# Performance work log

Measured on AMD Instinct MI355X. Metric: run time of the kernel, lower is better.

## Reference

```python
import jax, jax.numpy as jnp
import numpy as np
from jax import lax

B, C, FH, FW = 2, 128, 96, 160
H, W = 384, 640
NH, NP = 4, 9
T = 0.5


def conv(x, w, b, groups=1):
    pad = w.shape[2] // 2
    y = lax.conv_general_dilated(x, w, (1, 1), [(pad, pad), (pad, pad)],
                                 dimension_numbers=('NCHW', 'OIHW', 'NCHW'),
                                 feature_group_count=groups)
    return y + b[None, :, None, None]


def lrelu(x):
    return jnp.where(x >= 0, x, 0.1 * x)


def resize(x, h, w):
    # torch F.interpolate(mode='bilinear', align_corners=False, antialias=False)
    return jax.image.resize(x, (x.shape[0], x.shape[1], h, w), method='linear', antialias=False)


def grid_sample(vals, gx, gy, align_corners):
    # vals: (N, Ch, Hv, Wv); gx, gy: (N, Ho, Wo) normalized coords in [-1, 1]
    # bilinear, padding_mode='border'
    N, Ch, Hv, Wv = vals.shape
    if align_corners:
        x = (gx + 1.0) * 0.5 * (Wv - 1)
        y = (gy + 1.0) * 0.5 * (Hv - 1)
    else:
        x = ((gx + 1.0) * Wv - 1.0) * 0.5
        y = ((gy + 1.0) * Hv - 1.0) * 0.5
    x = jnp.clip(x, 0.0, Wv - 1.0)
    y = jnp.clip(y, 0.0, Hv - 1.0)
    x0 = jnp.floor(x)
    y0 = jnp.floor(y)
    wx = (x - x0)[:, None]  # (N,1,Ho,Wo)
    wy = (y - y0)[:, None]
    x0i = x0.astype(jnp.int32)
    y0i = y0.astype(jnp.int32)
    x1i = jnp.minimum(x0i + 1, Wv - 1)
    y1i = jnp.minimum(y0i + 1, Hv - 1)
    flat = vals.reshape(N, Ch, Hv * Wv)
    gather = jax.vmap(lambda v, i: jnp.take(v, i, axis=1))  # (Ch,HW),(Ho,Wo)->(Ch,Ho,Wo)
    v00 = gather(flat, y0i * Wv + x0i)
    v01 = gather(flat, y0i * Wv + x1i)
    v10 = gather(flat, y1i * Wv + x0i)
    v11 = gather(flat, y1i * Wv + x1i)
    return (v00 * (1 - wx) * (1 - wy) + v01 * wx * (1 - wy)
            + v10 * (1 - wx) * wy + v11 * wx * wy)


def warp(feat, flow):
    b, c, h, w = feat.shape
    if flow.shape[2:] != (h, w):
        sh, sw = h / flow.shape[2], w / flow.shape[3]
        flow = resize(flow, h, w) * jnp.array([sw, sh], flow.dtype)[None, :, None, None]
    gy, gx = jnp.meshgrid(jnp.arange(h, dtype=jnp.float32),
                          jnp.arange(w, dtype=jnp.float32), indexing='ij')
    gxn = 2.0 * (gx[None] + flow[:, 0]) / max(w - 1, 1) - 1.0
    gyn = 2.0 * (gy[None] + flow[:, 1]) / max(h - 1, 1) - 1.0
    return grid_sample(feat, gxn, gyn, True)


def group_norm(x, g, b, groups=8, eps=1e-5):
    B_, C_, h, w = x.shape
    xr = x.reshape(B_, groups, C_ // groups, h, w)
    m = xr.mean(axis=(2, 3, 4), keepdims=True)
    v = xr.var(axis=(2, 3, 4), keepdims=True)
    xn = ((xr - m) * lax.rsqrt(v + eps)).reshape(B_, C_, h, w)
    return xn * g[None, :, None, None] + b[None, :, None, None]


def deform_attn(q, src, ow0, ob0, ow1, ob1, aw0, ab0, aw1, ab1, vw, vb, pw, pb):
    b, c, h, w = q.shape
    hd = c // NH
    off = conv(lrelu(conv(q, ow0, ob0, groups=NH)), ow1, ob1).reshape(b, NH, NP, 2, h, w)
    attn = conv(lrelu(conv(q, aw0, ab0, groups=NH)), aw1, ab1).reshape(b, NH, NP, h, w)
    attn = jax.nn.softmax(attn, axis=2)
    vals = conv(src, vw, vb).reshape(b * NH, hd, h, w)
    gy, gx = jnp.meshgrid(jnp.arange(h, dtype=jnp.float32),
                          jnp.arange(w, dtype=jnp.float32), indexing='ij')
    sx = gx[None, None, None] + off[:, :, :, 0]  # (b,NH,NP,h,w)
    sy = gy[None, None, None] + off[:, :, :, 1]
    gxn = (2.0 * sx / max(w - 1, 1) - 1.0).reshape(b * NH, NP * h, w)
    gyn = (2.0 * sy / max(h - 1, 1) - 1.0).reshape(b * NH, NP * h, w)
    samp = grid_sample(vals, gxn, gyn, False).reshape(b, NH, hd, NP, h, w)
    out = (samp * attn[:, :, None]).sum(axis=3).reshape(b, c, h, w)
    return conv(out, pw, pb)


def setup_inputs() -> dict:
    key = jax.random.key(0)
    ks = jax.random.split(key, 24)
    rn = lambda k, s, sc: jax.random.normal(k, s, jnp.float32) * sc
    # offset conv bias: 3x3 regular grid init (n_points=9), padded with zeros
    gs = 3
    base = []
    for dy in range(gs):
        for dx in range(gs):
            base += [dx - gs // 2, dy - gs // 2]
    ob1 = np.zeros(NH * NP * 2, np.float32)
    ob1[:len(base)] = np.asarray(base, np.float32)
    return {
        'feat1': rn(ks[0], (B, C, FH, FW), 1.0),
        'feat2': rn(ks[1], (B, C, FH, FW), 1.0),
        'flow_fwd': rn(ks[2], (B, 2, H, W), 3.0),
        'flow_bwd': rn(ks[3], (B, 2, H, W), 3.0),
        'edge1': jax.random.uniform(ks[4], (B, 1, H, W), jnp.float32),
        'edge2': jax.random.uniform(ks[5], (B, 1, H, W), jnp.float32),
        'fuse_w0': rn(ks[6], (C, 2 * C + 3, 3, 3), 0.02),
        'fuse_b0': jnp.zeros((C,), jnp.float32),
        'fuse_w1': rn(ks[7], (C, C, 3, 3), 0.02),
        'fuse_b1': jnp.zeros((C,), jnp.float32),
        'gn_g': jnp.ones((C,), jnp.float32),
        'gn_b': jnp.zeros((C,), jnp.float32),
        'off_w0': rn(ks[8], (C, C // NH, 3, 3), 0.02),
        'off_b0': jnp.zeros((C,), jnp.float32),
        'off_w1': rn(ks[9], (NH * NP * 2, C, 1, 1), 0.01),
        'off_b1': jnp.asarray(ob1),
        'aw_w0': rn(ks[10], (C, C // NH, 3, 3), 0.02),
        'aw_b0': jnp.zeros((C,), jnp.float32),
        'aw_w1': rn(ks[11], (NH * NP, C, 1, 1), 0.02),
        'aw_b1': jnp.zeros((NH * NP,), jnp.float32),
        'val_w': rn(ks[12], (C, C, 1, 1), 0.05),
        'val_b': jnp.zeros((C,), jnp.float32),
        'out_w': rn(ks[13], (C, C, 1, 1), 0.05),
        'out_b': jnp.zeros((C,), jnp.float32),
        'ffn_w0': rn(ks[14], (2 * C, C, 1, 1), 0.05),
        'ffn_b0': jnp.zeros((2 * C,), jnp.float32),
        'ffn_w1': rn(ks[15], (C, 2 * C, 1, 1), 0.05),
        'ffn_b1': jnp.zeros((C,), jnp.float32),
        'dec_w0': rn(ks[16], (64, C, 3, 3), 0.03),
        'dec_b0': jnp.zeros((64,), jnp.float32),
        'dec_w1': rn(ks[17], (32, 64, 3, 3), 0.05),
        'dec_b1': jnp.zeros((32,), jnp.float32),
        'dec_w2': rn(ks[18], (3, 32, 3, 3), 0.05),
        'dec_b2': jnp.zeros((3,), jnp.float32),
    }


def reference(feat1, feat2, flow_fwd, flow_bwd, edge1, edge2,
              fuse_w0, fuse_b0, fuse_w1, fuse_b1, gn_g, gn_b,
              off_w0, off_b0, off_w1, off_b1, aw_w0, aw_b0, aw_w1, aw_b1,
              val_w, val_b, out_w, out_b, ffn_w0, ffn_b0, ffn_w1, ffn_b1,
              dec_w0, dec_b0, dec_w1, dec_b1, dec_w2, dec_b2):
    b, c, fh, fw = feat1.shape
    h, w = edge1.shape[2], edge1.shape[3]
    f1w = warp(feat1, flow_fwd * T)
    f2w = warp(feat2, flow_bwd * (1.0 - T))
    e1 = resize(edge1, fh, fw)
    e2 = resize(edge2, fh, fw)
    tmap = jnp.full((b, 1, fh, fw), T, feat1.dtype)
    fused = jnp.concatenate([f1w, f2w, e1, e2, tmap], axis=1)
    x = lrelu(conv(lrelu(conv(fused, fuse_w0, fuse_b0)), fuse_w1, fuse_b1))
    source = f1w * (1.0 - T) + f2w * T
    x = x + deform_attn(group_norm(x, gn_g, gn_b), source,
                        off_w0, off_b0, off_w1, off_b1,
                        aw_w0, aw_b0, aw_w1, aw_b1,
                        val_w, val_b, out_w, out_b)
    x = x + conv(jax.nn.gelu(conv(x, ffn_w0, ffn_b0), approximate=False), ffn_w1, ffn_b1)
    x = resize(x, h, w)
    x = lrelu(conv(x, dec_w0, dec_b0))
    x = lrelu(conv(x, dec_w1, dec_b1))
    return jax.nn.sigmoid(conv(x, dec_w2, dec_b2))
```

## Files before the change

kernel.cpp:

```cpp
#include <hip/hip_runtime.h>

typedef _Float16 f16;
typedef _Float16 f16x8 __attribute__((ext_vector_type(8)));
typedef float f32x4 __attribute__((ext_vector_type(4)));

constexpr int Bn = 2, Cn = 128, FH = 96, FW = 160, Hh = 384, Wh = 640;
constexpr int HWl = FH * FW;
constexpr int NHd = 4, NPt = 9;

#define DEVINL __device__ __forceinline__

DEVINL f32x4 zero4() { f32x4 z; z[0] = 0.f; z[1] = 0.f; z[2] = 0.f; z[3] = 0.f; return z; }
DEVINL f16x8 zero8() {
  f16x8 z;
#pragma unroll
  for (int j = 0; j < 8; ++j) z[j] = (f16)0.f;
  return z;
}

template<int ACT> DEVINL float activ(float v) {
  if (ACT == 1) return v >= 0.f ? v : 0.1f * v;
  if (ACT == 2) return 0.5f * v * (1.f + erff(v * 0.70710678118654752f));
  if (ACT == 3) return 1.f / (1.f + expf(-v));
  return v;
}

struct PrepJob { const float* w; f16* wf; int Cout, cin_g, cout_g, KS, CoF, taps, blk0; };
struct PrepArgs { PrepJob j[12]; };

__global__ __launch_bounds__(256) void k_wprep_all(PrepArgs a)
{
  int jb = 0;
#pragma unroll
  for (int t = 1; t < 12; ++t) if ((int)blockIdx.x >= a.j[t].blk0) jb = t;
  PrepJob J = a.j[jb];
  int idx = (blockIdx.x - J.blk0) * 256 + threadIdx.x;
  int total = J.taps * J.KS * J.CoF * 64;
  if (idx >= total) return;
  int lane = idx & 63;
  int rest = idx >> 6;
  int cf = rest % J.CoF;
  int rest2 = rest / J.CoF;
  int ks = rest2 % J.KS;
  int tap = rest2 / J.KS;
  int co = cf * 16 + (lane & 15);
  f16x8 v = zero8();
#pragma unroll
  for (int j = 0; j < 8; ++j) {
    int cip = ks * 32 + (lane >> 4) * 8 + j;
    int cil = cip - (co / J.cout_g) * J.cin_g;
    float x = 0.f;
    if (co < J.Cout && cil >= 0 && cil < J.cin_g)
      x = J.w[((size_t)co * J.cin_g + cil) * J.taps + tap];
    v[j] = (f16)x;
  }
  *(f16x8*)&J.wf[(size_t)idx * 8] = v;
}

__global__ __launch_bounds__(256) void k_tr_h(
    const float* __restrict__ feat1, const float* __restrict__ feat2,
    f16* __restrict__ t1, f16* __restrict__ t2)
{
  int idx = blockIdx.x * blockDim.x + threadIdx.x;
  if (idx >= 2 * Bn * HWl * 8) return;
  int cq = idx & 7;
  int pix = (idx >> 3) % HWl;
  int z = idx / (8 * HWl);
  int b = z & 1;
  const float* src = (z >> 1) ? feat2 : feat1;
  f16* dst = (z >> 1) ? t2 : t1;
  int c0 = cq * 16;
  f16x8 v0, v1;
#pragma unroll
  for (int j = 0; j < 8; ++j) {
    v0[j] = (f16)src[(size_t)(b * Cn + c0 + j) * HWl + pix];
    v1[j] = (f16)src[(size_t)(b * Cn + c0 + 8 + j) * HWl + pix];
  }
  f16* dp = dst + ((size_t)b * HWl + pix) * 128 + c0;
  *(f16x8*)dp = v0;
  *(f16x8*)(dp + 8) = v1;
}

__global__ __launch_bounds__(256) void k_warp_fuse_h(
    const f16* __restrict__ t1, const f16* __restrict__ t2,
    const float* __restrict__ flowf, const float* __restrict__ flowb,
    const float* __restrict__ edge1, const float* __restrict__ edge2,
    f16* __restrict__ fused, f16* __restrict__ src)
{
  int idx = blockIdx.x * blockDim.x + threadIdx.x;
  if (idx >= Bn * HWl * 8) return;
  int cq = idx & 7;
  int pix = (idx >> 3) % HWl;
  int b = idx / (8 * HWl);
  int j = pix % FW;
  int i = pix / FW;

  const int y4 = 4 * i + 1, x4 = 4 * j + 1;
  const float* p;
  p = flowf + (size_t)((b * 2 + 0) * Hh + y4) * Wh + x4;
  float fx1 = 0.03125f * (p[0] + p[1] + p[Wh] + p[Wh + 1]);
  p = flowf + (size_t)((b * 2 + 1) * Hh + y4) * Wh + x4;
  float fy1 = 0.03125f * (p[0] + p[1] + p[Wh] + p[Wh + 1]);
  p = flowb + (size_t)((b * 2 + 0) * Hh + y4) * Wh + x4;
  float fx2 = 0.03125f * (p[0] + p[1] + p[Wh] + p[Wh + 1]);
  p = flowb + (size_t)((b * 2 + 1) * Hh + y4) * Wh + x4;
  float fy2 = 0.03125f * (p[0] + p[1] + p[Wh] + p[Wh + 1]);

  float sx1 = fminf(fmaxf((float)j + fx1, 0.f), (float)(FW - 1));
  float sy1 = fminf(fmaxf((float)i + fy1, 0.f), (float)(FH - 1));
  float sx2 = fminf(fmaxf((float)j + fx2, 0.f), (float)(FW - 1));
  float sy2 = fminf(fmaxf((float)i + fy2, 0.f), (float)(FH - 1));

  int x10 = (int)floorf(sx1), y10 = (int)floorf(sy1);
  int x11 = min(x10 + 1, FW - 1), y11 = min(y10 + 1, FH - 1);
  float wx1 = sx1 - (float)x10, wy1 = sy1 - (float)y10;
  int x20 = (int)floorf(sx2), y20 = (int)floorf(sy2);
  int x21 = min(x20 + 1, FW - 1), y21 = min(y20 + 1, FH - 1);
  float wx2 = sx2 - (float)x20, wy2 = sy2 - (float)y20;

  float a00 = (1.f - wx1) * (1.f - wy1), a01 = wx1 * (1.f - wy1);
  float a10 = (1.f - wx1) * wy1,         a11 = wx1 * wy1;
  float c00 = (1.f - wx2) * (1.f - wy2), c01 = wx2 * (1.f - wy2);
  float c10 = (1.f - wx2) * wy2,         c11 = wx2 * wy2;

  int c0 = cq * 16;
  const f16* b1 = t1 + (size_t)b * HWl * 128 + c0;
  const f16* b2 = t2 + (size_t)b * HWl * 128 + c0;
  const f16x8* p100 = (const f16x8*)&b1[(size_t)(y10 * FW + x10) * 128];
  const f16x8* p101 = (const f16x8*)&b1[(size_t)(y10 * FW + x11) * 128];
  const f16x8* p110 = (const f16x8*)&b1[(size_t)(y11 * FW + x10) * 128];
  const f16x8* p111 = (const f16x8*)&b1[(size_t)(y11 * FW + x11) * 128];
  const f16x8* p200 = (const f16x8*)&b2[(size_t)(y20 * FW + x20) * 128];
  const f16x8* p201 = (const f16x8*)&b2[(size_t)(y20 * FW + x21) * 128];
  const f16x8* p210 = (const f16x8*)&b2[(size_t)(y21 * FW + x20) * 128];
  const f16x8* p211 = (const f16x8*)&b2[(size_t)(y21 * FW + x21) * 128];

  f16* fp = fused + ((size_t)b * HWl + pix) * 288;
  f16* sp = src + ((size_t)b * HWl + pix) * 128;

#pragma unroll
  for (int h = 0; h < 2; ++h) {
    f16x8 u00 = p100[h], u01 = p101[h], u10 = p110[h], u11 = p111[h];
    f16x8 w00 = p200[h], w01 = p201[h], w10 = p210[h], w11 = p211[h];
    f16x8 r1, r2, rs;
#pragma unroll
    for (int k = 0; k < 8; ++k) {
      float v1 = (float)u00[k] * a00 + (float)u01[k] * a01
               + (float)u10[k] * a10 + (float)u11[k] * a11;
      float v2 = (float)w00[k] * c00 + (float)w01[k] * c01
               + (float)w10[k] * c10 + (float)w11[k] * c11;
      r1[k] = (f16)v1; r2[k] = (f16)v2; rs[k] = (f16)(0.5f * (v1 + v2));
    }
    *(f16x8*)(fp + c0 + h * 8) = r1;
    *(f16x8*)(fp + 128 + c0 + h * 8) = r2;
    *(f16x8*)(sp + c0 + h * 8) = rs;
  }

  if (cq == 0) {
    p = edge1 + (size_t)(b * Hh + y4) * Wh + x4;
    float e1v = 0.25f * (p[0] + p[1] + p[Wh] + p[Wh + 1]);
    p = edge2 + (size_t)(b * Hh + y4) * Wh + x4;
    float e2v = 0.25f * (p[0] + p[1] + p[Wh] + p[Wh + 1]);
    fp[256] = (f16)e1v;
    fp[257] = (f16)e2v;
    fp[258] = (f16)0.5f;
#pragma unroll
    for (int c = 259; c < 288; ++c) fp[c] = (f16)0.f;
  }
}

template<int ACT, int UP, int NF>
__global__ __launch_bounds__(256) void k_conv3m(
    const f16* __restrict__ Xin, const f16* __restrict__ Wf,
    const float* __restrict__ bias, f16* __restrict__ Out,
    int KS, int CoF, int Cs_in, int Cs_out, int Wd, int Ht,
    int in_r0, int in_rows, int out_r0, int out_rows, int ogr0, int ogr1)
{
  __shared__ f16 sA[8160];
  int tid = threadIdx.x;
  int wv = tid >> 6, lane = tid & 63;
  int l15 = lane & 15, l4 = lane >> 4;
  int colTiles = Wd >> 5;
  int tileC = blockIdx.x % colTiles, tileR = blockIdx.x / colTiles;
  int b = blockIdx.z;
  int co0 = blockIdx.y * (NF * 16);
  int cfB = blockIdx.y * NF;
  int rowBaseOut = ogr0 + tileR * 4;
  int rowBase = rowBaseOut - 1;
  int colBase = tileC * 32;

  f32x4 acc[2][NF];
#pragma unroll
  for (int mf = 0; mf < 2; ++mf)
#pragma unroll
    for (int nf = 0; nf < NF; ++nf) acc[mf][nf] = zero4();

  f16x8 stv[4];
  f16x8 stc[4][4];

  auto prefetch = [&](int cs) {
#pragma unroll
    for (int k = 0; k < 4; ++k) {
      int u = tid + k * 256;
      if (u < 816) {
        int s = u & 3;
        int pxy = u >> 2;
        int x = pxy % 34, y = pxy / 34;
        int gy = rowBase + y, gx = colBase + x - 1;
        if (UP) {
          stc[k][0] = zero8(); stc[k][1] = zero8();
          stc[k][2] = zero8(); stc[k][3] = zero8();
          if (gy >= 0 && gy < Ht && gx >= 0 && gx < Wd) {
            float uy = ((float)gy + 0.5f) * 0.25f - 0.5f;
            uy = fminf(fmaxf(uy, 0.f), (float)(FH - 1));
            int y0 = (int)floorf(uy);
            int y1 = min(y0 + 1, FH - 1);
            float ux = ((float)gx + 0.5f) * 0.25f - 0.5f;
            ux = fminf(fmaxf(ux, 0.f), (float)(FW - 1));
            int x0 = (int)floorf(ux);
            int x1 = min(x0 + 1, FW - 1);
            const f16* xb = Xin + (size_t)b * HWl * 128 + cs * 32 + s * 8;
            stc[k][0] = *(const f16x8*)&xb[(size_t)(y0 * FW + x0) * 128];
            stc[k][1] = *(const f16x8*)&xb[(size_t)(y0 * FW + x1) * 128];
            stc[k][2] = *(const f16x8*)&xb[(size_t)(y1 * FW + x0) * 128];
            stc[k][3] = *(const f16x8*)&xb[(size_t)(y1 * FW + x1) * 128];
          }
        } else {
          stv[k] = zero8();
          if (gy >= in_r0 && gy < in_r0 + in_rows && gx >= 0 && gx < Wd)
            stv[k] = *(const f16x8*)&Xin[(((size_t)b * in_rows + (gy - in_r0)) * Wd + gx) * Cs_in
                                         + cs * 32 + s * 8];
        }
      }
    }
  };

  auto writeLDS = [&]() {
#pragma unroll
    for (int k = 0; k < 4; ++k) {
      int u = tid + k * 256;
      if (u < 816) {
        int s = u & 3;
        int pxy = u >> 2;
        f16x8 v;
        if (UP) {
          int x = pxy % 34, y = pxy / 34;
          int gy = rowBase + y, gx = colBase + x - 1;
          float uy = ((float)gy + 0.5f) * 0.25f - 0.5f;
          uy = fminf(fmaxf(uy, 0.f), (float)(FH - 1));
          float fy = uy - floorf(uy);
          float ux = ((float)gx + 0.5f) * 0.25f - 0.5f;
          ux = fminf(fmaxf(ux, 0.f), (float)(FW - 1));
          float fx = ux - floorf(ux);
#pragma unroll
          for (int jj = 0; jj < 8; ++jj) {
            float t0 = (float)stc[k][0][jj] * (1.f - fx) + (float)stc[k][1][jj] * fx;
            float t1 = (float)stc[k][2][jj] * (1.f - fx) + (float)stc[k][3][jj] * fx;
            v[jj] = (f16)(t0 * (1.f - fy) + t1 * fy);
          }
        } else {
          v = stv[k];
        }
        *(f16x8*)((char*)sA + pxy * 80 + s * 16) = v;
      }
    }
  };

  prefetch(0);
  for (int cs = 0; cs < KS; ++cs) {
    writeLDS();
    __syncthreads();
    if (cs + 1 < KS) prefetch(cs + 1);
#pragma unroll
    for (int ky = 0; ky < 3; ++ky) {
#pragma unroll
      for (int kx = 0; kx < 3; ++kx) {
        const char* ab = (const char*)sA;
        f16x8 a0 = *(const f16x8*)(ab + ((wv + ky) * 34 + l15 + kx) * 80 + l4 * 16);
        f16x8 a1 = *(const f16x8*)(ab + ((wv + ky) * 34 + l15 + 16 + kx) * 80 + l4 * 16);
        int tap = ky * 3 + kx;
#pragma unroll
        for (int nf = 0; nf < NF; ++nf) {
          f16x8 bf = *(const f16x8*)&Wf[((((size_t)tap * KS + cs) * CoF + cfB + nf) * 64 + lane) * 8];
          acc[0][nf] = __builtin_amdgcn_mfma_f32_16x16x32_f16(a0, bf, acc[0][nf], 0, 0, 0);
          acc[1][nf] = __builtin_amdgcn_mfma_f32_16x16x32_f16(a1, bf, acc[1][nf], 0, 0, 0);
        }
      }
    }
    __syncthreads();
  }

  int r = rowBaseOut + wv;
  if (r < ogr1) {
    size_t rowoff = ((size_t)b * out_rows + (r - out_r0)) * Wd;
#pragma unroll
    for (int nf = 0; nf < NF; ++nf) {
      int co = co0 + nf * 16 + l15;
      float bv = bias[co];
#pragma unroll
      for (int mf = 0; mf < 2; ++mf) {
        int xo = colBase + mf * 16 + l4 * 4;
#pragma unroll
        for (int rg = 0; rg < 4; ++rg) {
          float v = activ<ACT>(acc[mf][nf][rg] + bv);
          Out[(rowoff + xo + rg) * Cs_out + co] = (f16)v;
        }
      }
    }
  }
}

template<int ACT, int RES>
__global__ __launch_bounds__(256) void k_gemm1x1(
    const f16* __restrict__ X, const f16* __restrict__ Wf,
    const float* __restrict__ bias, f16* __restrict__ Out,
    int KS, int CoF, int Cs_in, int Cs_out, int Cr, int coTiles, int pixTiles)
{
  int wid = blockIdx.x * 4 + (threadIdx.x >> 6);
  int lane = threadIdx.x & 63;
  int total = pixTiles * coTiles;
  if (wid >= total) return;
  int coT = wid % coTiles;
  int pixT = wid / coTiles;
  int nfc = min(4, CoF - coT * 4);
  int l15 = lane & 15, l4 = lane >> 4;

  f32x4 acc[2][4];
#pragma unroll
  for (int mf = 0; mf < 2; ++mf)
#pragma unroll
    for (int nf = 0; nf < 4; ++nf) acc[mf][nf] = zero4();

  int pA0 = pixT * 32 + l15;
  for (int ks = 0; ks < KS; ++ks) {
    f16x8 a0 = *(const f16x8*)&X[(size_t)pA0 * Cs_in + ks * 32 + l4 * 8];
    f16x8 a1 = *(const f16x8*)&X[(size_t)(pA0 + 16) * Cs_in + ks * 32 + l4 * 8];
#pragma unroll
    for (int nf = 0; nf < 4; ++nf) {
      if (nf < nfc) {
        f16x8 bf = *(const f16x8*)&Wf[(((size_t)ks * CoF + coT * 4 + nf) * 64 + lane) * 8];
        acc[0][nf] = __builtin_amdgcn_mfma_f32_16x16x32_f16(a0, bf, acc[0][nf], 0, 0, 0);
        acc[1][nf] = __builtin_amdgcn_mfma_f32_16x16x32_f16(a1, bf, acc[1][nf], 0, 0, 0);
      }
    }
  }
#pragma unroll
  for (int nf = 0; nf < 4; ++nf) {
    if (nf < nfc) {
      int co = coT * 64 + nf * 16 + l15;
      if (co < Cr) {
        float bv = bias[co];
#pragma unroll
        for (int mf = 0; mf < 2; ++mf) {
          int p0 = pixT * 32 + mf * 16 + l4 * 4;
#pragma unroll
          for (int rg = 0; rg < 4; ++rg) {
            float v = activ<ACT>(acc[mf][nf][rg] + bv);
            size_t o = (size_t)(p0 + rg) * Cs_out + co;
            if (RES) v += (float)Out[o];
            Out[o] = (f16)v;
          }
        }
      }
    }
  }
}

__global__ __launch_bounds__(256) void k_gn_part_h(
    const f16* __restrict__ X, float* __restrict__ part)
{
  int s = blockIdx.x & 7;
  int g = (blockIdx.x >> 3) & 7;
  int b = blockIdx.x >> 6;
  int tid = threadIdx.x;
  const f16* Xp = X + (size_t)b * HWl * 128 + g * 16 + (tid & 1) * 8;
  float sum = 0.f, ss = 0.f;
  for (int p = s * 1920 + (tid >> 1); p < (s + 1) * 1920; p += 128) {
    f16x8 v = *(const f16x8*)&Xp[(size_t)p * 128];
#pragma unroll
    for (int jj = 0; jj < 8; ++jj) { float f = (float)v[jj]; sum += f; ss += f * f; }
  }
  __shared__ float sh1[256], sh2[256];
  sh1[tid] = sum; sh2[tid] = ss;
  __syncthreads();
  for (int st = 128; st > 0; st >>= 1) {
    if (tid < st) { sh1[tid] += sh1[tid + st]; sh2[tid] += sh2[tid + st]; }
    __syncthreads();
  }
  if (tid == 0) {
    part[((b * 8 + g) * 8 + s) * 2] = sh1[0];
    part[((b * 8 + g) * 8 + s) * 2 + 1] = sh2[0];
  }
}

__global__ __launch_bounds__(256) void k_gn_apply_h(
    const f16* __restrict__ X, const float* __restrict__ gw,
    const float* __restrict__ gb, const float* __restrict__ part,
    f16* __restrict__ Q)
{
  int idx = blockIdx.x * blockDim.x + threadIdx.x;
  int total = Bn * HWl * 16;
  if (idx >= total) return;
  int u = idx & 15;
  int pix = (idx >> 4) % HWl;
  int b = idx / (16 * HWl);
  int c0 = u * 8;
  int g = c0 >> 4;
  const float* pp = part + ((b * 8 + g) * 8) * 2;
  float sum = 0.f, ss = 0.f;
#pragma unroll
  for (int s = 0; s < 8; ++s) { sum += pp[s * 2]; ss += pp[s * 2 + 1]; }
  const float n = 16.f * HWl;
  float mean = sum / n;
  float var = ss / n - mean * mean;
  float inv = rsqrtf(var + 1e-5f);
  f16x8 v = *(const f16x8*)&X[((size_t)b * HWl + pix) * 128 + c0];
  f16x8 r;
#pragma unroll
  for (int jj = 0; jj < 8; ++jj) {
    int c = c0 + jj;
    r[jj] = (f16)(((float)v[jj] - mean) * (gw[c] * inv) + gb[c]);
  }
  *(f16x8*)&Q[((size_t)b * HWl + pix) * 128 + c0] = r;
}

__global__ __launch_bounds__(256) void k_softmax9_h(f16* __restrict__ a)
{
  int idx = blockIdx.x * blockDim.x + threadIdx.x;
  if (idx >= Bn * NHd * HWl) return;
  int pix = idx % HWl;
  int head = (idx / HWl) & 3;
  int b = idx / (HWl * NHd);
  f16* base = a + ((size_t)b * HWl + pix) * 48 + head * 9;
  float v[9];
  float m = -1e30f;
#pragma unroll
  for (int p0 = 0; p0 < 9; ++p0) { v[p0] = (float)base[p0]; m = fmaxf(m, v[p0]); }
  float s = 0.f;
#pragma unroll
  for (int p0 = 0; p0 < 9; ++p0) { v[p0] = expf(v[p0] - m); s += v[p0]; }
  float inv = 1.f / s;
#pragma unroll
  for (int p0 = 0; p0 < 9; ++p0) base[p0] = (f16)(v[p0] * inv);
}

__global__ __launch_bounds__(256) void k_deform_h(
    const f16* __restrict__ vals, const f16* __restrict__ off,
    const f16* __restrict__ attn, f16* __restrict__ outa)
{
  int idx = blockIdx.x * blockDim.x + threadIdx.x;
  if (idx >= Bn * NHd * HWl) return;
  int pix = idx % HWl;
  int head = (idx / HWl) & 3;
  int b = idx / (HWl * NHd);
  int j = pix % FW, i = pix / FW;

  const float kx = (float)FW / (float)(FW - 1);
  const float ky = (float)FH / (float)(FH - 1);
  const f16* vb = vals + (size_t)b * HWl * 128 + head * 32;
  const f16* ab = attn + ((size_t)b * HWl + pix) * 48 + head * 9;
  const f16* ob = off + ((size_t)b * HWl + pix) * 80 + head * 18;

  float acc[32];
#pragma unroll
  for (int k = 0; k < 32; ++k) acc[k] = 0.f;

#pragma unroll
  for (int p0 = 0; p0 < 9; ++p0) {
    float ox = (float)ob[p0 * 2];
    float oy = (float)ob[p0 * 2 + 1];
    float aw = (float)ab[p0];
    float xf = ((float)j + ox) * kx - 0.5f;
    float yf = ((float)i + oy) * ky - 0.5f;
    xf = fminf(fmaxf(xf, 0.f), (float)(FW - 1));
    yf = fminf(fmaxf(yf, 0.f), (float)(FH - 1));
    int x0 = (int)floorf(xf), y0 = (int)floorf(yf);
    int x1 = min(x0 + 1, FW - 1), y1 = min(y0 + 1, FH - 1);
    float fx = xf - (float)x0, fy = yf - (float)y0;
    float w00 = aw * (1.f - fx) * (1.f - fy);
    float w01 = aw * fx * (1.f - fy);
    float w10 = aw * (1.f - fx) * fy;
    float w11 = aw * fx * fy;
    const f16x8* c00 = (const f16x8*)&vb[(size_t)(y0 * FW + x0) * 128];
    const f16x8* c01 = (const f16x8*)&vb[(size_t)(y0 * FW + x1) * 128];
    const f16x8* c10 = (const f16x8*)&vb[(size_t)(y1 * FW + x0) * 128];
    const f16x8* c11 = (const f16x8*)&vb[(size_t)(y1 * FW + x1) * 128];
#pragma unroll
    for (int k8 = 0; k8 < 4; ++k8) {
      f16x8 a = c00[k8], bb = c01[k8], cc = c10[k8], dd = c11[k8];
#pragma unroll
      for (int jj = 0; jj < 8; ++jj)
        acc[k8 * 8 + jj] += w00 * (float)a[jj] + w01 * (float)bb[jj]
                          + w10 * (float)cc[jj] + w11 * (float)dd[jj];
    }
  }
  f16* op = outa + ((size_t)b * HWl + pix) * 128 + head * 32;
#pragma unroll
  for (int k = 0; k < 32; ++k) op[k] = (f16)acc[k];
}

__global__ __launch_bounds__(256) void k_dec2_h(
    const f16* __restrict__ Xb, const float* __restrict__ w,
    const float* __restrict__ bias, float* __restrict__ out,
    int c0, int b0, int brows, int R)
{
  int idx = blockIdx.x * blockDim.x + threadIdx.x;
  if (idx >= Bn * R * Wh) return;
  int x = idx % Wh;
  int y = c0 + (idx / Wh) % R;
  int b = idx / (Wh * R);
  float a0 = bias[0], a1 = bias[1], a2 = bias[2];
#pragma unroll
  for (int ky = 0; ky < 3; ++ky) {
    int gy = y + ky - 1;
    if (gy < 0 || gy >= Hh) continue;
#pragma unroll
    for (int kxx = 0; kxx < 3; ++kxx) {
      int gx = x + kxx - 1;
      if (gx < 0 || gx >= Wh) continue;
      int tap = ky * 3 + kxx;
      const f16* px = Xb + ((size_t)(b * brows + (gy - b0)) * Wh + gx) * 32;
#pragma unroll
      for (int k8 = 0; k8 < 4; ++k8) {
        f16x8 v = *(const f16x8*)&px[k8 * 8];
#pragma unroll
        for (int jj = 0; jj < 8; ++jj) {
          int ci = k8 * 8 + jj;
          float f = (float)v[jj];
          a0 += f * w[(0 * 32 + ci) * 9 + tap];
          a1 += f * w[(1 * 32 + ci) * 9 + tap];
          a2 += f * w[(2 * 32 + ci) * 9 + tap];
        }
      }
    }
  }
  size_t o = ((size_t)(b * 3 + 0) * Hh + y) * Wh + x;
  out[o] = 1.f / (1.f + expf(-a0));
  out[o + (size_t)Hh * Wh] = 1.f / (1.f + expf(-a1));
  out[o + (size_t)2 * Hh * Wh] = 1.f / (1.f + expf(-a2));
}

extern "C" void kernel_launch(void* const* d_in, const int* in_sizes, int n_in,
                              void* d_out, int out_size, void* d_ws, size_t ws_size,
                              hipStream_t stream) {
  (void)in_sizes; (void)n_in; (void)out_size; (void)ws_size;
  const float* feat1  = (const float*)d_in[0];
  const float* feat2  = (const float*)d_in[1];
  const float* flowf  = (const float*)d_in[2];
  const float* flowb  = (const float*)d_in[3];
  const float* edge1  = (const float*)d_in[4];
  const float* edge2  = (const float*)d_in[5];
  const float* fuse_w0 = (const float*)d_in[6];
  const float* fuse_b0 = (const float*)d_in[7];
  const float* fuse_w1 = (const float*)d_in[8];
  const float* fuse_b1 = (const float*)d_in[9];
  const float* gn_g   = (const float*)d_in[10];
  const float* gn_b   = (const float*)d_in[11];
  const float* off_w0 = (const float*)d_in[12];
  const float* off_b0 = (const float*)d_in[13];
  const float* off_w1 = (const float*)d_in[14];
  const float* off_b1 = (const float*)d_in[15];
  const float* aw_w0  = (const float*)d_in[16];
  const float* aw_b0  = (const float*)d_in[17];
  const float* aw_w1  = (const float*)d_in[18];
  const float* aw_b1  = (const float*)d_in[19];
  const float* val_w  = (const float*)d_in[20];
  const float* val_b  = (const float*)d_in[21];
  const float* out_w  = (const float*)d_in[22];
  const float* out_b  = (const float*)d_in[23];
  const float* ffn_w0 = (const float*)d_in[24];
  const float* ffn_b0 = (const float*)d_in[25];
  const float* ffn_w1 = (const float*)d_in[26];
  const float* ffn_b1 = (const float*)d_in[27];
  const float* dec_w0 = (const float*)d_in[28];
  const float* dec_b0 = (const float*)d_in[29];
  const float* dec_w1 = (const float*)d_in[30];
  const float* dec_b1 = (const float*)d_in[31];
  const float* dec_w2 = (const float*)d_in[32];
  const float* dec_b2 = (const float*)d_in[33];
  float* out = (float*)d_out;

  f16* ws16 = (f16*)d_ws;
  size_t o = 0;
  auto alloc = [&](size_t n) { f16* p = ws16 + o; o += (n + 7) & ~(size_t)7; return p; };
  f16* xbuf  = alloc((size_t)2 * HWl * 128);
  f16* pool  = alloc((size_t)0);
  f16* regA  = alloc((size_t)2 * HWl * 288);
  f16* regB  = alloc((size_t)2 * HWl * 128);
  f16* regC  = alloc((size_t)2 * HWl * 128);
  f16* offb  = alloc((size_t)2 * HWl * 80);
  f16* attnb = alloc((size_t)2 * HWl * 48);
  f16* regF  = alloc((size_t)2 * HWl * 131);
  f16* featT1 = alloc((size_t)2 * HWl * 128);
  f16* featT2 = alloc((size_t)2 * HWl * 128);
  f16* wfF0 = alloc(9 * 288 * 128);
  f16* wfF1 = alloc(9 * 128 * 128);
  f16* wfO0 = alloc(9 * 128 * 128);
  f16* wfA0 = alloc(9 * 128 * 128);
  f16* wfD0 = alloc(9 * 128 * 64);
  f16* wfD1 = alloc(9 * 64 * 32);
  f16* w1O  = alloc(4 * 5 * 512);
  f16* w1A  = alloc(4 * 3 * 512);
  f16* w1V  = alloc(4 * 8 * 512);
  f16* w1U  = alloc(4 * 8 * 512);
  f16* w1G0 = alloc(4 * 16 * 512);
  f16* w1G1 = alloc(8 * 8 * 512);
  float* gnp = (float*)alloc(512);

  f16* fused = regA;
  f16* t_off = regA;
  f16* t_aw  = regA;
  f16* ffn_t = regA;
  f16* src_h = regB;
  f16* out_attn = regB;
  f16* tmp_h = regC;
  f16* qb    = regC;
  f16* valsb = regF;
  f16* bufA  = pool;
  f16* bufB  = pool + (size_t)2 * 196 * 640 * 64;

  dim3 blk(256);
  auto pg = [](long n) { return dim3((unsigned)((n + 255) / 256)); };

  PrepArgs pa;
  int pb = 0;
  auto addj = [&](int k, const float* w, f16* wf, int Cout, int cing, int coutg,
                  int KS, int CoF, int taps) {
    pa.j[k] = PrepJob{w, wf, Cout, cing, coutg, KS, CoF, taps, pb};
    pb += (taps * KS * CoF * 64 + 255) / 256;
  };
  addj(0, fuse_w0, wfF0, 128, 259, 128, 9, 8, 9);
  addj(1, fuse_w1, wfF1, 128, 128, 128, 4, 8, 9);
  addj(2, off_w0, wfO0, 128, 32, 32, 4, 8, 9);
  addj(3, aw_w0,  wfA0, 128, 32, 32, 4, 8, 9);
  addj(4, dec_w0, wfD0, 64, 128, 64, 4, 4, 9);
  addj(5, dec_w1, wfD1, 32, 64, 32, 2, 2, 9);
  addj(6, off_w1, w1O, 72, 128, 128, 4, 5, 1);
  addj(7, aw_w1,  w1A, 36, 128, 128, 4, 3, 1);
  addj(8, val_w,  w1V, 128, 128, 128, 4, 8, 1);
  addj(9, out_w,  w1U, 128, 128, 128, 4, 8, 1);
  addj(10, ffn_w0, w1G0, 256, 128, 128, 4, 16, 1);
  addj(11, ffn_w1, w1G1, 128, 256, 256, 8, 8, 1);
  pa.j[6].cin_g = 128;  pa.j[6].cout_g = 72;
  pa.j[7].cin_g = 128;  pa.j[7].cout_g = 36;
  pa.j[8].cin_g = 128;  pa.j[8].cout_g = 128;
  pa.j[9].cin_g = 128;  pa.j[9].cout_g = 128;
  pa.j[10].cin_g = 128; pa.j[10].cout_g = 256;
  pa.j[11].cin_g = 256; pa.j[11].cout_g = 128;
  k_wprep_all<<<dim3((unsigned)pb), blk, 0, stream>>>(pa);

  k_tr_h<<<pg(2L * Bn * HWl * 8), blk, 0, stream>>>(feat1, feat2, featT1, featT2);
  k_warp_fuse_h<<<pg((long)Bn * HWl * 8), blk, 0, stream>>>(featT1, featT2, flowf, flowb,
                                                            edge1, edge2, fused, src_h);
  dim3 gF(24 * 5, 2, 2);
  k_conv3m<1, 0, 4><<<gF, blk, 0, stream>>>(fused, wfF0, fuse_b0, tmp_h,
      9, 8, 288, 128, FW, FH, 0, FH, 0, FH, 0, FH);
  k_conv3m<1, 0, 4><<<gF, blk, 0, stream>>>(tmp_h, wfF1, fuse_b1, xbuf,
      4, 8, 128, 128, FW, FH, 0, FH, 0, FH, 0, FH);
  k_gn_part_h<<<dim3(128), blk, 0, stream>>>(xbuf, gnp);
  k_gn_apply_h<<<pg(2L * HWl * 16), blk, 0, stream>>>(xbuf, gn_g, gn_b, gnp, qb);
  k_conv3m<1, 0, 4><<<gF, blk, 0, stream>>>(qb, wfO0, off_b0, t_off,
      4, 8, 128, 128, FW, FH, 0, FH, 0, FH, 0, FH);
  k_gemm1x1<0, 0><<<dim3(480), blk, 0, stream>>>(t_off, w1O, off_b1, offb,
      4, 5, 128, 80, 72, 2, 960);
  k_conv3m<1, 0, 4><<<gF, blk, 0, stream>>>(qb, wfA0, aw_b0, t_aw,
      4, 8, 128, 128, FW, FH, 0, FH, 0, FH, 0, FH);
  k_gemm1x1<0, 0><<<dim3(240), blk, 0, stream>>>(t_aw, w1A, aw_b1, attnb,
      4, 3, 128, 48, 36, 1, 960);
  k_softmax9_h<<<pg(2L * NHd * HWl), blk, 0, stream>>>(attnb);
  k_gemm1x1<0, 0><<<dim3(480), blk, 0, stream>>>(src_h, w1V, val_b, valsb,
      4, 8, 128, 128, 128, 2, 960);
  k_deform_h<<<pg(2L * NHd * HWl), blk, 0, stream>>>(valsb, offb, attnb, out_attn);
  k_gemm1x1<0, 1><<<dim3(480), blk, 0, stream>>>(out_attn, w1U, out_b, xbuf,
      4, 8, 128, 128, 128, 2, 960);
  k_gemm1x1<2, 0><<<dim3(960), blk, 0, stream>>>(xbuf, w1G0, ffn_b0, ffn_t,
      4, 16, 128, 256, 256, 4, 960);
  k_gemm1x1<0, 1><<<dim3(480), blk, 0, stream>>>(ffn_t, w1G1, ffn_b1, xbuf,
      8, 8, 256, 128, 128, 2, 960);

  for (int c0 = 0; c0 < Hh; c0 += 192) {
    int c1 = c0 + 192;
    int a0 = c0 - 2 > 0 ? c0 - 2 : 0;
    int a1 = c1 + 2 < Hh ? c1 + 2 : Hh;
    int b0 = c0 - 1 > 0 ? c0 - 1 : 0;
    int b1 = c1 + 1 < Hh ? c1 + 1 : Hh;
    int ar = a1 - a0, br = b1 - b0;
    dim3 gD0((unsigned)(((ar + 3) / 4) * 20), 1, 2);
    k_conv3m<1, 1, 4><<<gD0, blk, 0, stream>>>(xbuf, wfD0, dec_b0, bufA,
        4, 4, 128, 64, Wh, Hh, 0, 0, a0, ar, a0, a1);
    dim3 gD1((unsigned)(((br + 3) / 4) * 20), 1, 2);
    k_conv3m<1, 0, 2><<<gD1, blk, 0, stream>>>(bufA, wfD1, dec_b1, bufB,
        2, 2, 64, 32, Wh, Hh, a0, ar, b0, br, b0, b1);
    k_dec2_h<<<pg(2L * 192 * Wh), blk, 0, stream>>>(bufB, dec_w2, dec_b2, out,
                                                    c0, b0, br, 192);
  }
}
```

Baseline: 610.5 us.

## Replace LDS-tiled 3x3 conv with per-wave direct-load MFMA conv and fuse offset/attn convs

The shared-memory tiled 3x3 convolution is replaced by a kernel where each wavefront reads its A fragments straight from global memory (relying on cache) and computes an M×NF block of MFMA tiles, with no LDS staging or block barriers. The offset and attention-weight 3x3 convs are merged into a single launch with 256 output channels, using the weight-prep packing offset and a split bias. The decoder's upsample, previously done inside the conv prefetch, becomes a separate kernel writing a full-resolution buffer, and the decoder chunk size drops from 192 to 96 rows to fit workspace. This trades LDS data reuse and fused upsampling for simpler, barrier-free kernels and fewer launches, at the cost of more global/L2 traffic and an extra materialized upsampled buffer.

```diff
diff --git a/kernel.cpp b/kernel.cpp
--- a/kernel.cpp
+++ b/kernel.cpp
@@ -25,7 +25,7 @@
   return v;
 }
 
-struct PrepJob { const float* w; f16* wf; int Cout, cin_g, cout_g, KS, CoF, taps, blk0; };
+struct PrepJob { const float* w; f16* wf; int Cout, cin_g, cout_g, KS, CoF, taps, CoFt, cf0, blk0; };
 struct PrepArgs { PrepJob j[12]; };
 
 __global__ __launch_bounds__(256) void k_wprep_all(PrepArgs a)
@@ -54,7 +54,8 @@
       x = J.w[((size_t)co * J.cin_g + cil) * J.taps + tap];
     v[j] = (f16)x;
   }
-  *(f16x8*)&J.wf[(size_t)idx * 8] = v;
+  size_t oidx = (((size_t)tap * J.KS + ks) * J.CoFt + J.cf0 + cf) * 64 + lane;
+  *(f16x8*)&J.wf[oidx * 8] = v;
 }
 
 __global__ __launch_bounds__(256) void k_tr_h(
@@ -169,144 +170,122 @@
   }
 }
 
-template<int ACT, int UP, int NF>
-__global__ __launch_bounds__(256) void k_conv3m(
-    const f16* __restrict__ Xin, const f16* __restrict__ Wf,
-    const float* __restrict__ bias, f16* __restrict__ Out,
-    int KS, int CoF, int Cs_in, int Cs_out, int Wd, int Ht,
-    int in_r0, int in_rows, int out_r0, int out_rows, int ogr0, int ogr1)
-{
-  __shared__ f16 sA[8160];
-  int tid = threadIdx.x;
-  int wv = tid >> 6, lane = tid & 63;
+template<int ACT, int M, int NF, int W>
+__global__ __launch_bounds__(256) void k_conv3g(
+    const f16* __restrict__ X, const f16* __restrict__ Wf,
+    const float* __restrict__ bias, const float* __restrict__ bias2, int bsplit,
+    f16* __restrict__ Out,
+    int KS, int CoF, int Cs_in, int Cs_out, int Htot,
+    int in_r0, int in_rows, int out_r0, int out_rows,
+    int ogr0, int nrows, int coTiles)
+{
+  int wid = blockIdx.x * 4 + (threadIdx.x >> 6);
+  int lane = threadIdx.x & 63;
   int l15 = lane & 15, l4 = lane >> 4;
-  int colTiles = Wd >> 5;
-  int tileC = blockIdx.x % colTiles, tileR = blockIdx.x / colTiles;
+  int pixTiles = nrows * W / (M * 16);
+  if (wid >= pixTiles * coTiles) return;
+  int coT = wid % coTiles;
+  int pixT = wid / coTiles;
   int b = blockIdx.z;
-  int co0 = blockIdx.y * (NF * 16);
-  int cfB = blockIdx.y * NF;
-  int rowBaseOut = ogr0 + tileR * 4;
-  int rowBase = rowBaseOut - 1;
-  int colBase = tileC * 32;
-
-  f32x4 acc[2][NF];
-#pragma unroll
-  for (int mf = 0; mf < 2; ++mf)
+  int base = pixT * (M * 16);
+  int row = ogr0 + base / W;
+  int colB = base % W;
+
+  f32x4 acc[M][NF];
+#pragma unroll
+  for (int mf = 0; mf < M; ++mf)
 #pragma unroll
     for (int nf = 0; nf < NF; ++nf) acc[mf][nf] = zero4();
 
-  f16x8 stv[4];
-  f16x8 stc[4][4];
-
-  auto prefetch = [&](int cs) {
-#pragma unroll
-    for (int k = 0; k < 4; ++k) {
-      int u = tid + k * 256;
-      if (u < 816) {
-        int s = u & 3;
-        int pxy = u >> 2;
-        int x = pxy % 34, y = pxy / 34;
-        int gy = rowBase + y, gx = colBase + x - 1;
-        if (UP) {
-          stc[k][0] = zero8(); stc[k][1] = zero8();
-          stc[k][2] = zero8(); stc[k][3] = zero8();
-          if (gy >= 0 && gy < Ht && gx >= 0 && gx < Wd) {
-            float uy = ((float)gy + 0.5f) * 0.25f - 0.5f;
-            uy = fminf(fmaxf(uy, 0.f), (float)(FH - 1));
-            int y0 = (int)floorf(uy);
-            int y1 = min(y0 + 1, FH - 1);
-            float ux = ((float)gx + 0.5f) * 0.25f - 0.5f;
-            ux = fminf(fmaxf(ux, 0.f), (float)(FW - 1));
-            int x0 = (int)floorf(ux);
-            int x1 = min(x0 + 1, FW - 1);
-            const f16* xb = Xin + (size_t)b * HWl * 128 + cs * 32 + s * 8;
-            stc[k][0] = *(const f16x8*)&xb[(size_t)(y0 * FW + x0) * 128];
-            stc[k][1] = *(const f16x8*)&xb[(size_t)(y0 * FW + x1) * 128];
-            stc[k][2] = *(const f16x8*)&xb[(size_t)(y1 * FW + x0) * 128];
-            stc[k][3] = *(const f16x8*)&xb[(size_t)(y1 * FW + x1) * 128];
-          }
-        } else {
-          stv[k] = zero8();
-          if (gy >= in_r0 && gy < in_r0 + in_rows && gx >= 0 && gx < Wd)
-            stv[k] = *(const f16x8*)&Xin[(((size_t)b * in_rows + (gy - in_r0)) * Wd + gx) * Cs_in
-                                         + cs * 32 + s * 8];
+  for (int cs = 0; cs < KS; ++cs) {
+#pragma unroll
+    for (int ky = 0; ky < 3; ++ky) {
+      int srow = row + ky - 1;
+      bool rv = (srow >= 0 && srow < Htot);
+      int crow = min(max(srow, in_r0), in_r0 + in_rows - 1);
+      const f16* rp = X + (((size_t)b * in_rows + (crow - in_r0)) * W) * (size_t)Cs_in
+                      + cs * 32 + l4 * 8;
+#pragma unroll
+      for (int kx = 0; kx < 3; ++kx) {
+        int tap = ky * 3 + kx;
+        f16x8 Bf[NF];
+#pragma unroll
+        for (int nf = 0; nf < NF; ++nf)
+          Bf[nf] = *(const f16x8*)&Wf[((((size_t)tap * KS + cs) * CoF + coT * NF + nf) * 64 + lane) * 8];
+        f16x8 Af[M];
+#pragma unroll
+        for (int mf = 0; mf < M; ++mf) {
+          int scol = colB + mf * 16 + l15 + kx - 1;
+          f16x8 a = zero8();
+          if (rv && (unsigned)scol < (unsigned)W)
+            a = *(const f16x8*)&rp[(size_t)scol * Cs_in];
+          Af[mf] = a;
         }
+#pragma unroll
+        for (int mf = 0; mf < M; ++mf)
+#pragma unroll
+          for (int nf = 0; nf < NF; ++nf)
+            acc[mf][nf] = __builtin_amdgcn_mfma_f32_16x16x32_f16(Af[mf], Bf[nf], acc[mf][nf], 0, 0, 0);
       }
     }
-  };
-
-  auto writeLDS = [&]() {
-#pragma unroll
-    for (int k = 0; k < 4; ++k) {
-      int u = tid + k * 256;
-      if (u < 816) {
-        int s = u & 3;
-        int pxy = u >> 2;
-        f16x8 v;
-        if (UP) {
-          int x = pxy % 34, y = pxy / 34;
-          int gy = rowBase + y, gx = colBase + x - 1;
-          float uy = ((float)gy + 0.5f) * 0.25f - 0.5f;
-          uy = fminf(fmaxf(uy, 0.f), (float)(FH - 1));
-          float fy = uy - floorf(uy);
-          float ux = ((float)gx + 0.5f) * 0.25f - 0.5f;
-          ux = fminf(fmaxf(ux, 0.f), (float)(FW - 1));
-          float fx = ux - floorf(ux);
-#pragma unroll
-          for (int jj = 0; jj < 8; ++jj) {
-            float t0 = (float)stc[k][0][jj] * (1.f - fx) + (float)stc[k][1][jj] * fx;
-            float t1 = (float)stc[k][2][jj] * (1.f - fx) + (float)stc[k][3][jj] * fx;
-            v[jj] = (f16)(t0 * (1.f - fy) + t1 * fy);
-          }
-        } else {
-          v = stv[k];
-        }
-        *(f16x8*)((char*)sA + pxy * 80 + s * 16) = v;
+  }
+
+  size_t rowoff = ((size_t)b * out_rows + (row - out_r0)) * W;
+#pragma unroll
+  for (int nf = 0; nf < NF; ++nf) {
+    int co = coT * (NF * 16) + nf * 16 + l15;
+    float bv = (co < bsplit) ? bias[co] : bias2[co - bsplit];
+#pragma unroll
+    for (int mf = 0; mf < M; ++mf) {
+      int xo = colB + mf * 16 + l4 * 4;
+#pragma unroll
+      for (int rg = 0; rg < 4; ++rg) {
+        float v = activ<ACT>(acc[mf][nf][rg] + bv);
+        Out[(rowoff + xo + rg) * (size_t)Cs_out + co] = (f16)v;
       }
     }
-  };
-
-  prefetch(0);
-  for (int cs = 0; cs < KS; ++cs) {
-    writeLDS();
-    __syncthreads();
-    if (cs + 1 < KS) prefetch(cs + 1);
-#pragma unroll
-    for (int ky = 0; ky < 3; ++ky) {
-#pragma unroll
-      for (int kx = 0; kx < 3; ++kx) {
-        const char* ab = (const char*)sA;
-        f16x8 a0 = *(const f16x8*)(ab + ((wv + ky) * 34 + l15 + kx) * 80 + l4 * 16);
-        f16x8 a1 = *(const f16x8*)(ab + ((wv + ky) * 34 + l15 + 16 + kx) * 80 + l4 * 16);
-        int tap = ky * 3 + kx;
-#pragma unroll
-        for (int nf = 0; nf < NF; ++nf) {
-          f16x8 bf = *(const f16x8*)&Wf[((((size_t)tap * KS + cs) * CoF + cfB + nf) * 64 + lane) * 8];
-          acc[0][nf] = __builtin_amdgcn_mfma_f32_16x16x32_f16(a0, bf, acc[0][nf], 0, 0, 0);
-          acc[1][nf] = __builtin_amdgcn_mfma_f32_16x16x32_f16(a1, bf, acc[1][nf], 0, 0, 0);
-        }
-      }
-    }
-    __syncthreads();
-  }
-
-  int r = rowBaseOut + wv;
-  if (r < ogr1) {
-    size_t rowoff = ((size_t)b * out_rows + (r - out_r0)) * Wd;
-#pragma unroll
-    for (int nf = 0; nf < NF; ++nf) {
-      int co = co0 + nf * 16 + l15;
-      float bv = bias[co];
-#pragma unroll
-      for (int mf = 0; mf < 2; ++mf) {
-        int xo = colBase + mf * 16 + l4 * 4;
-#pragma unroll
-        for (int rg = 0; rg < 4; ++rg) {
-          float v = activ<ACT>(acc[mf][nf][rg] + bv);
-          Out[(rowoff + xo + rg) * Cs_out + co] = (f16)v;
-        }
-      }
-    }
+  }
+}
+
+__global__ __launch_bounds__(256) void k_up4_h(
+    const f16* __restrict__ Xl, f16* __restrict__ U, int u0, int urows)
+{
+  int idx = blockIdx.x * blockDim.x + threadIdx.x;
+  if (idx >= Bn * urows * Wh * 8) return;
+  int cq = idx & 7;
+  int x = (idx >> 3) % Wh;
+  int r = ((idx >> 3) / Wh) % urows;
+  int b = idx / (8 * Wh * urows);
+  int R = u0 + r;
+
+  float uy = ((float)R + 0.5f) * 0.25f - 0.5f;
+  uy = fminf(fmaxf(uy, 0.f), (float)(FH - 1));
+  int y0 = (int)floorf(uy);
+  int y1 = min(y0 + 1, FH - 1);
+  float fy = uy - (float)y0;
+  float ux = ((float)x + 0.5f) * 0.25f - 0.5f;
+  ux = fminf(fmaxf(ux, 0.f), (float)(FW - 1));
+  int x0 = (int)floorf(ux);
+  int x1 = min(x0 + 1, FW - 1);
+  float fx = ux - (float)x0;
+
+  const f16* xb = Xl + (size_t)b * HWl * 128 + cq * 16;
+  const f16x8* c00 = (const f16x8*)&xb[(size_t)(y0 * FW + x0) * 128];
+  const f16x8* c01 = (const f16x8*)&xb[(size_t)(y0 * FW + x1) * 128];
+  const f16x8* c10 = (const f16x8*)&xb[(size_t)(y1 * FW + x0) * 128];
+  const f16x8* c11 = (const f16x8*)&xb[(size_t)(y1 * FW + x1) * 128];
+  f16* up = U + (((size_t)b * urows + r) * Wh + x) * 128 + cq * 16;
+#pragma unroll
+  for (int h = 0; h < 2; ++h) {
+    f16x8 a = c00[h], bb = c01[h], cc = c10[h], dd = c11[h];
+    f16x8 o;
+#pragma unroll
+    for (int jj = 0; jj < 8; ++jj) {
+      float t0 = (float)a[jj] * (1.f - fx) + (float)bb[jj] * fx;
+      float t1 = (float)cc[jj] * (1.f - fx) + (float)dd[jj] * fx;
+      o[jj] = (f16)(t0 * (1.f - fy) + t1 * fy);
+    }
+    *(f16x8*)(up + h * 8) = o;
   }
 }
 
@@ -584,7 +563,19 @@
   size_t o = 0;
   auto alloc = [&](size_t n) { f16* p = ws16 + o; o += (n + 7) & ~(size_t)7; return p; };
   f16* xbuf  = alloc((size_t)2 * HWl * 128);
-  f16* pool  = alloc((size_t)0);
+  f16* wfF0 = alloc(9 * 9 * 8 * 512);
+  f16* wfF1 = alloc(9 * 4 * 8 * 512);
+  f16* wfOA = alloc(9 * 4 * 16 * 512);
+  f16* wfD0 = alloc(9 * 4 * 4 * 512);
+  f16* wfD1 = alloc(9 * 2 * 2 * 512);
+  f16* w1O  = alloc(4 * 5 * 512);
+  f16* w1A  = alloc(4 * 3 * 512);
+  f16* w1V  = alloc(4 * 8 * 512);
+  f16* w1U  = alloc(4 * 8 * 512);
+  f16* w1G0 = alloc(4 * 16 * 512);
+  f16* w1G1 = alloc(8 * 8 * 512);
+  float* gnp = (float*)alloc(512);
+  f16* pool  = ws16 + o;
   f16* regA  = alloc((size_t)2 * HWl * 288);
   f16* regB  = alloc((size_t)2 * HWl * 128);
   f16* regC  = alloc((size_t)2 * HWl * 128);
@@ -593,80 +584,62 @@
   f16* regF  = alloc((size_t)2 * HWl * 131);
   f16* featT1 = alloc((size_t)2 * HWl * 128);
   f16* featT2 = alloc((size_t)2 * HWl * 128);
-  f16* wfF0 = alloc(9 * 288 * 128);
-  f16* wfF1 = alloc(9 * 128 * 128);
-  f16* wfO0 = alloc(9 * 128 * 128);
-  f16* wfA0 = alloc(9 * 128 * 128);
-  f16* wfD0 = alloc(9 * 128 * 64);
-  f16* wfD1 = alloc(9 * 64 * 32);
-  f16* w1O  = alloc(4 * 5 * 512);
-  f16* w1A  = alloc(4 * 3 * 512);
-  f16* w1V  = alloc(4 * 8 * 512);
-  f16* w1U  = alloc(4 * 8 * 512);
-  f16* w1G0 = alloc(4 * 16 * 512);
-  f16* w1G1 = alloc(8 * 8 * 512);
-  float* gnp = (float*)alloc(512);
 
   f16* fused = regA;
-  f16* t_off = regA;
-  f16* t_aw  = regA;
+  f16* t_oa  = regA;
   f16* ffn_t = regA;
   f16* src_h = regB;
   f16* out_attn = regB;
   f16* tmp_h = regC;
   f16* qb    = regC;
   f16* valsb = regF;
-  f16* bufA  = pool;
-  f16* bufB  = pool + (size_t)2 * 196 * 640 * 64;
+  f16* bufU = pool;
+  f16* bufA = bufU + (size_t)2 * 103 * 640 * 128;
+  f16* bufB = bufA + (size_t)2 * 100 * 640 * 64;
 
   dim3 blk(256);
   auto pg = [](long n) { return dim3((unsigned)((n + 255) / 256)); };
+  auto cg = [](int pixTiles, int coTiles) {
+    return dim3((unsigned)((pixTiles * coTiles + 3) / 4), 1, 2);
+  };
+  const int BIG = 1 << 30;
 
   PrepArgs pa;
   int pb = 0;
   auto addj = [&](int k, const float* w, f16* wf, int Cout, int cing, int coutg,
-                  int KS, int CoF, int taps) {
-    pa.j[k] = PrepJob{w, wf, Cout, cing, coutg, KS, CoF, taps, pb};
+                  int KS, int CoF, int taps, int CoFt, int cf0) {
+    pa.j[k] = PrepJob{w, wf, Cout, cing, coutg, KS, CoF, taps, CoFt, cf0, pb};
     pb += (taps * KS * CoF * 64 + 255) / 256;
   };
-  addj(0, fuse_w0, wfF0, 128, 259, 128, 9, 8, 9);
-  addj(1, fuse_w1, wfF1, 128, 128, 128, 4, 8, 9);
-  addj(2, off_w0, wfO0, 128, 32, 32, 4, 8, 9);
-  addj(3, aw_w0,  wfA0, 128, 32, 32, 4, 8, 9);
-  addj(4, dec_w0, wfD0, 64, 128, 64, 4, 4, 9);
-  addj(5, dec_w1, wfD1, 32, 64, 32, 2, 2, 9);
-  addj(6, off_w1, w1O, 72, 128, 128, 4, 5, 1);
-  addj(7, aw_w1,  w1A, 36, 128, 128, 4, 3, 1);
-  addj(8, val_w,  w1V, 128, 128, 128, 4, 8, 1);
-  addj(9, out_w,  w1U, 128, 128, 128, 4, 8, 1);
-  addj(10, ffn_w0, w1G0, 256, 128, 128, 4, 16, 1);
-  addj(11, ffn_w1, w1G1, 128, 256, 256, 8, 8, 1);
-  pa.j[6].cin_g = 128;  pa.j[6].cout_g = 72;
-  pa.j[7].cin_g = 128;  pa.j[7].cout_g = 36;
-  pa.j[8].cin_g = 128;  pa.j[8].cout_g = 128;
-  pa.j[9].cin_g = 128;  pa.j[9].cout_g = 128;
-  pa.j[10].cin_g = 128; pa.j[10].cout_g = 256;
-  pa.j[11].cin_g = 256; pa.j[11].cout_g = 128;
+  addj(0, fuse_w0, wfF0, 128, 259, 128, 9, 8, 9, 8, 0);
+  addj(1, fuse_w1, wfF1, 128, 128, 128, 4, 8, 9, 8, 0);
+  addj(2, off_w0, wfOA, 128, 32, 32, 4, 8, 9, 16, 0);
+  addj(3, aw_w0,  wfOA, 128, 32, 32, 4, 8, 9, 16, 8);
+  addj(4, dec_w0, wfD0, 64, 128, 64, 4, 4, 9, 4, 0);
+  addj(5, dec_w1, wfD1, 32, 64, 32, 2, 2, 9, 2, 0);
+  addj(6, off_w1, w1O, 72, 128, 72, 4, 5, 1, 5, 0);
+  addj(7, aw_w1,  w1A, 36, 128, 36, 4, 3, 1, 3, 0);
+  addj(8, val_w,  w1V, 128, 128, 128, 4, 8, 1, 8, 0);
+  addj(9, out_w,  w1U, 128, 128, 128, 4, 8, 1, 8, 0);
+  addj(10, ffn_w0, w1G0, 256, 128, 256, 4, 16, 1, 16, 0);
+  addj(11, ffn_w1, w1G1, 128, 256, 128, 8, 8, 1, 8, 0);
   k_wprep_all<<<dim3((unsigned)pb), blk, 0, stream>>>(pa);
 
   k_tr_h<<<pg(2L * Bn * HWl * 8), blk, 0, stream>>>(feat1, feat2, featT1, featT2);
   k_warp_fuse_h<<<pg((long)Bn * HWl * 8), blk, 0, stream>>>(featT1, featT2, flowf, flowb,
                                                             edge1, edge2, fused, src_h);
-  dim3 gF(24 * 5, 2, 2);
-  k_conv3m<1, 0, 4><<<gF, blk, 0, stream>>>(fused, wfF0, fuse_b0, tmp_h,
-      9, 8, 288, 128, FW, FH, 0, FH, 0, FH, 0, FH);
-  k_conv3m<1, 0, 4><<<gF, blk, 0, stream>>>(tmp_h, wfF1, fuse_b1, xbuf,
-      4, 8, 128, 128, FW, FH, 0, FH, 0, FH, 0, FH);
+  k_conv3g<1, 2, 2, 160><<<cg(480, 4), blk, 0, stream>>>(fused, wfF0, fuse_b0, fuse_b0, BIG,
+      tmp_h, 9, 8, 288, 128, FH, 0, FH, 0, FH, 0, FH, 4);
+  k_conv3g<1, 2, 2, 160><<<cg(480, 4), blk, 0, stream>>>(tmp_h, wfF1, fuse_b1, fuse_b1, BIG,
+      xbuf, 4, 8, 128, 128, FH, 0, FH, 0, FH, 0, FH, 4);
   k_gn_part_h<<<dim3(128), blk, 0, stream>>>(xbuf, gnp);
   k_gn_apply_h<<<pg(2L * HWl * 16), blk, 0, stream>>>(xbuf, gn_g, gn_b, gnp, qb);
-  k_conv3m<1, 0, 4><<<gF, blk, 0, stream>>>(qb, wfO0, off_b0, t_off,
-      4, 8, 128, 128, FW, FH, 0, FH, 0, FH, 0, FH);
-  k_gemm1x1<0, 0><<<dim3(480), blk, 0, stream>>>(t_off, w1O, off_b1, offb,
-      4, 5, 128, 80, 72, 2, 960);
-  k_conv3m<1, 0, 4><<<gF, blk, 0, stream>>>(qb, wfA0, aw_b0, t_aw,
-      4, 8, 128, 128, FW, FH, 0, FH, 0, FH, 0, FH);
-  k_gemm1x1<0, 0><<<dim3(240), blk, 0, stream>>>(t_aw, w1A, aw_b1, attnb,
-      4, 3, 128, 48, 36, 1, 960);
+  k_conv3g<1, 2, 2, 160><<<cg(480, 8), blk, 0, stream>>>(qb, wfOA, off_b0, aw_b0, 128,
+      t_oa, 4, 16, 128, 256, FH, 0, FH, 0, FH, 0, FH, 8);
+  k_gemm1x1<0, 0><<<dim3(480), blk, 0, stream>>>(t_oa, w1O, off_b1, offb,
+      4, 5, 256, 80, 72, 2, 960);
+  k_gemm1x1<0, 0><<<dim3(240), blk, 0, stream>>>(t_oa + 128, w1A, aw_b1, attnb,
+      4, 3, 256, 48, 36, 1, 960);
   k_softmax9_h<<<pg(2L * NHd * HWl), blk, 0, stream>>>(attnb);
   k_gemm1x1<0, 0><<<dim3(480), blk, 0, stream>>>(src_h, w1V, val_b, valsb,
       4, 8, 128, 128, 128, 2, 960);
@@ -678,20 +651,21 @@
   k_gemm1x1<0, 1><<<dim3(480), blk, 0, stream>>>(ffn_t, w1G1, ffn_b1, xbuf,
       8, 8, 256, 128, 128, 2, 960);
 
-  for (int c0 = 0; c0 < Hh; c0 += 192) {
-    int c1 = c0 + 192;
+  for (int c0 = 0; c0 < Hh; c0 += 96) {
+    int c1 = c0 + 96;
     int a0 = c0 - 2 > 0 ? c0 - 2 : 0;
     int a1 = c1 + 2 < Hh ? c1 + 2 : Hh;
     int b0 = c0 - 1 > 0 ? c0 - 1 : 0;
     int b1 = c1 + 1 < Hh ? c1 + 1 : Hh;
-    int ar = a1 - a0, br = b1 - b0;
-    dim3 gD0((unsigned)(((ar + 3) / 4) * 20), 1, 2);
-    k_conv3m<1, 1, 4><<<gD0, blk, 0, stream>>>(xbuf, wfD0, dec_b0, bufA,
-        4, 4, 128, 64, Wh, Hh, 0, 0, a0, ar, a0, a1);
-    dim3 gD1((unsigned)(((br + 3) / 4) * 20), 1, 2);
-    k_conv3m<1, 0, 2><<<gD1, blk, 0, stream>>>(bufA, wfD1, dec_b1, bufB,
-        2, 2, 64, 32, Wh, Hh, a0, ar, b0, br, b0, b1);
-    k_dec2_h<<<pg(2L * 192 * Wh), blk, 0, stream>>>(bufB, dec_w2, dec_b2, out,
-                                                    c0, b0, br, 192);
-  }
-}
+    int u0 = a0 - 1 > 0 ? a0 - 1 : 0;
+    int u1 = a1 + 1 < Hh ? a1 + 1 : Hh;
+    int ar = a1 - a0, br = b1 - b0, ur = u1 - u0;
+    k_up4_h<<<pg(2L * ur * Wh * 8), blk, 0, stream>>>(xbuf, bufU, u0, ur);
+    k_conv3g<1, 4, 4, 640><<<cg(ar * 10, 1), blk, 0, stream>>>(bufU, wfD0, dec_b0, dec_b0, BIG,
+        bufA, 4, 4, 128, 64, Hh, u0, ur, a0, ar, a0, ar, 1);
+    k_conv3g<1, 4, 2, 640><<<cg(br * 10, 1), blk, 0, stream>>>(bufA, wfD1, dec_b1, dec_b1, BIG,
+        bufB, 2, 2, 64, 32, Hh, a0, ar, b0, br, b0, br, 1);
+    k_dec2_h<<<pg(2L * 96 * Wh), blk, 0, stream>>>(bufB, dec_w2, dec_b2, out,
+                                                   c0, b0, br, 96);
+  }
+}
```

New measurement: 785.7 us. 1.29x slower.
